# Kernel tuning notes

Measured on AMD Instinct MI355X. Metric: run time of the kernel, lower is better.

## Reference

```python
import jax, jax.numpy as jnp
import numpy as np

N_NODES = 100000
N_EDGES = 3200000
N_FEAT = 128
N_GRAPHS = 1024
N_CLASSES = 10
K = 30  # global_sort_pool k


def setup_inputs() -> dict:
    key = jax.random.key(0)
    ks = jax.random.split(key, 20)
    p = lambda k, shape: jax.random.normal(k, shape, jnp.float32) * 0.1
    return {
        "x": jax.random.normal(ks[0], (N_NODES, N_FEAT), jnp.float32),
        "w1": p(ks[1], (N_FEAT, 32)), "b1": p(ks[2], (32,)),
        "w2": p(ks[3], (32, 32)),     "b2": p(ks[4], (32,)),
        "w3": p(ks[5], (32, 32)),     "b3": p(ks[6], (32,)),
        "w4": p(ks[7], (32, 1)),      "b4": p(ks[8], (1,)),
        "conv5_w": p(ks[9], (16, 1, 97)),  "conv5_b": p(ks[10], (16,)),
        "conv6_w": p(ks[11], (32, 16, 5)), "conv6_b": p(ks[12], (32,)),
        "fc1_w": p(ks[13], (352, 128)),    "fc1_b": p(ks[14], (128,)),
        "fc2_w": p(ks[15], (128, N_CLASSES)), "fc2_b": p(ks[16], (N_CLASSES,)),
        "edge_src": jax.random.randint(ks[17], (N_EDGES,), 0, N_NODES),
        "edge_dst": jax.random.randint(ks[18], (N_EDGES,), 0, N_NODES),
        "batch": jnp.sort(jax.random.randint(ks[19], (N_NODES,), 0, N_GRAPHS)),
        "num_graphs": N_GRAPHS,
    }


def _gcn_forward(x, w1, b1, w2, b2, w3, b3, w4, b4,
                 conv5_w, conv5_b, conv6_w, conv6_b,
                 fc1_w, fc1_b, fc2_w, fc2_b,
                 edge_src, edge_dst, batch, num_graphs):
    n = x.shape[0]
    # remove_self_loops: mask self-loop edges to weight 0 (shapes stay static)
    ew = (edge_src != edge_dst).astype(x.dtype)
    # gcn_norm with added self-loops (weight 1): deg includes self-loop
    deg = jax.ops.segment_sum(ew, edge_dst, num_segments=n) + 1.0
    dis = jax.lax.rsqrt(deg)                       # deg^{-1/2}
    enorm = dis[edge_src] * dis[edge_dst] * ew     # [E]
    snorm = (dis * dis)[:, None]                   # self-loop norm [n,1]

    def gcn_conv(h, W, b):
        h = h @ W                                   # [n, out]
        agg = jax.ops.segment_sum(h[edge_src] * enorm[:, None], edge_dst,
                                  num_segments=n) + h * snorm
        return agg + b

    x1 = jnp.tanh(gcn_conv(x,  w1, b1))   # [n,32]
    x2 = jnp.tanh(gcn_conv(x1, w2, b2))   # [n,32]
    x3 = jnp.tanh(gcn_conv(x2, w3, b3))   # [n,32]
    x4 = jnp.tanh(gcn_conv(x3, w4, b4))   # [n,1]
    xc = jnp.concatenate([x1, x2, x3, x4], axis=-1)  # [n,97]

    # global_sort_pool(k=K): per-graph sort by last channel, descending
    key_last = xc[:, -1]
    order = jnp.lexsort((-key_last, batch))          # primary: batch, secondary: desc key
    bs = batch[order]                                # sorted graph ids
    counts = jax.ops.segment_sum(jnp.ones_like(batch, jnp.int32), batch,
                                 num_segments=num_graphs)
    starts = jnp.cumsum(counts) - counts             # exclusive prefix sum
    rank = jnp.arange(n) - starts[bs]                # rank within own graph
    r = jnp.where(rank < K, rank, K)                 # overflow -> dummy slot K
    pooled = jnp.zeros((num_graphs, K + 1, 97), xc.dtype)
    pooled = pooled.at[bs, r].set(xc[order])
    pooled = pooled[:, :K, :].reshape(num_graphs, 1, K * 97)  # [B,1,2910]

    # Conv1d(1,16,97,97) + relu
    h = jax.lax.conv_general_dilated(pooled, conv5_w, (97,), 'VALID',
                                     dimension_numbers=('NCH', 'OIH', 'NCH'))
    h = jax.nn.relu(h + conv5_b[None, :, None])      # [B,16,30]
    # MaxPool1d(2,2)
    h = jax.lax.reduce_window(h, -jnp.inf, jax.lax.max,
                              (1, 1, 2), (1, 1, 2), 'VALID')  # [B,16,15]
    # Conv1d(16,32,5,1) + relu
    h = jax.lax.conv_general_dilated(h, conv6_w, (1,), 'VALID',
                                     dimension_numbers=('NCH', 'OIH', 'NCH'))
    h = jax.nn.relu(h + conv6_b[None, :, None])      # [B,32,11]
    h = h.reshape(num_graphs, -1)                    # [B,352]

    h = jax.nn.relu(h @ fc1_w + fc1_b)               # [B,128]; dropout = identity (eval)
    return jax.nn.log_softmax(h @ fc2_w + fc2_b, axis=-1)  # [B,num_classes]


def reference(x, w1, b1, w2, b2, w3, b3, w4, b4,
              conv5_w, conv5_b, conv6_w, conv6_b,
              fc1_w, fc1_b, fc2_w, fc2_b,
              edge_src, edge_dst, batch, num_graphs):
    return _gcn_forward(x, w1, b1, w2, b2, w3, b3, w4, b4,
                        conv5_w, conv5_b, conv6_w, conv6_b,
                        fc1_w, fc1_b, fc2_w, fc2_b,
                        edge_src, edge_dst, batch, num_graphs)
```

## Files before the change

kernel.cpp:

```cpp
#include <hip/hip_runtime.h>
#include <hip/hip_bf16.h>

#define N_NODES 100000
#define N_EDGES 3200000
#define NGRAPH 1024
#define KTOP 30

#define NBKT 782
#define NTILE 391
#define TILE 8192
#define BKT_CAP 4736
#define GMAX 512

typedef __hip_bfloat16 bf16;
typedef float vfloat4 __attribute__((ext_vector_type(4)));

__device__ __forceinline__ float u2f(unsigned short h) {
    return __uint_as_float(((unsigned int)h) << 16);
}
__device__ __forceinline__ float LD(const void* p, int i, int bf) {
    if (bf) return u2f(((const unsigned short*)p)[i]);
    return ((const float*)p)[i];
}

__global__ void k_detect(const void* w1, int* flag) {
    if (threadIdx.x == 0 && blockIdx.x == 0) {
        const unsigned short* u = (const unsigned short*)w1;
        int plausible = 0;
        for (int i = 0; i < 64; i++) {
            float a = fabsf(u2f(u[2 * i]));
            if (a == 0.f || (a >= 9.765625e-4f && a <= 2.0f)) plausible++;
        }
        *flag = (plausible >= 40) ? 1 : 0;
    }
}

__global__ void k_icur(int* __restrict__ cur) {
    int i = blockIdx.x * 256 + threadIdx.x;
    if (i < NBKT) cur[i] = i * BKT_CAP;
}

__global__ __launch_bounds__(256) void k_scat(const int* __restrict__ src,
                                              const int* __restrict__ dst,
                                              int* __restrict__ cur,
                                              int* __restrict__ ebuf) {
    __shared__ int h[NBKT];
    __shared__ int base[NBKT];
    int tid = threadIdx.x;
    int ebase = blockIdx.x * TILE;
    for (int i = tid; i < NBKT; i += 256) h[i] = 0;
    __syncthreads();
    for (int i = tid; i < TILE; i += 256) {
        int e = ebase + i;
        if (e < N_EDGES) {
            int s = src[e], d = dst[e];
            if (s != d) atomicAdd(&h[d >> 7], 1);
        }
    }
    __syncthreads();
    for (int i = tid; i < NBKT; i += 256) {
        int c = h[i];
        base[i] = c ? atomicAdd(&cur[i], c) : 0;
    }
    __syncthreads();
    for (int i = tid; i < NBKT; i += 256) h[i] = 0;
    __syncthreads();
    for (int i = tid; i < TILE; i += 256) {
        int e = ebase + i;
        if (e < N_EDGES) {
            int s = src[e], d = dst[e];
            if (s != d) {
                int bkt = d >> 7;
                int p = base[bkt] + atomicAdd(&h[bkt], 1);
                if (p < (bkt + 1) * BKT_CAP) ebuf[p] = ((d & 127) << 17) | s;
            }
        }
    }
}

__global__ __launch_bounds__(256) void k_bcnt(const int* __restrict__ ebuf,
                                              const int* __restrict__ cur,
                                              int* __restrict__ rs,
                                              int* __restrict__ re,
                                              float* __restrict__ dis,
                                              int* __restrict__ deg) {
    __shared__ int dloc[128];
    __shared__ int sc[128];
    int b = blockIdx.x;
    int node0 = b << 7;
    int nn = N_NODES - node0; if (nn > 128) nn = 128;
    int tid = threadIdx.x;
    if (tid < 128) dloc[tid] = 0;
    __syncthreads();
    int s = b * BKT_CAP;
    int cnt = cur[b] - s; if (cnt > BKT_CAP) cnt = BKT_CAP;
    int e = s + cnt;
    for (int i = s + tid; i < e; i += 256)
        atomicAdd(&dloc[ebuf[i] >> 17], 1);
    __syncthreads();
    if (tid < 128) sc[tid] = dloc[tid];
    __syncthreads();
    for (int off = 1; off < 128; off <<= 1) {
        int t = (tid >= off && tid < 128) ? sc[tid - off] : 0;
        __syncthreads();
        if (tid < 128) sc[tid] += t;
        __syncthreads();
    }
    if (tid < nn) {
        int st = s + sc[tid] - dloc[tid];
        rs[node0 + tid] = st;
        re[node0 + tid] = st + dloc[tid];
        dis[node0 + tid] = rsqrtf((float)dloc[tid] + 1.0f);
        deg[node0 + tid] = dloc[tid];
    }
}

__global__ __launch_bounds__(256) void k_bfill(const int* __restrict__ ebuf,
                                               const int* __restrict__ cur,
                                               const int* __restrict__ rs,
                                               const int* __restrict__ deg,
                                               int* __restrict__ csr) {
    __shared__ int cl[128];
    int b = blockIdx.x;
    int node0 = b << 7;
    int tid = threadIdx.x;
    if (tid < 128) {
        int n = node0 + tid;
        cl[tid] = (n < N_NODES) ? rs[n] : 0;
    }
    __syncthreads();
    int s = b * BKT_CAP;
    int cnt = cur[b] - s; if (cnt > BKT_CAP) cnt = BKT_CAP;
    int e = s + cnt;
    for (int i = s + tid; i < e; i += 256) {
        int pv = ebuf[i];
        int srcn = pv & 0x1FFFF;
        int pos = atomicAdd(&cl[pv >> 17], 1);
        int d = deg[srcn];
        csr[pos] = (d << 17) | srcn;
    }
}

__global__ void k_gstart(const int* __restrict__ batch, int* __restrict__ gstart) {
    int g = blockIdx.x * 256 + threadIdx.x;
    if (g > NGRAPH) return;
    int lo = 0, hi = N_NODES;
    while (lo < hi) {
        int mid = (lo + hi) >> 1;
        if (batch[mid] < g) lo = mid + 1; else hi = mid;
    }
    gstart[g] = lo;
}

#define MM1_B 64
__global__ __launch_bounds__(256) void k_mm1(const void* __restrict__ x,
                                             const void* __restrict__ w,
                                             const int* __restrict__ flagp,
                                             const float* __restrict__ dis,
                                             float* __restrict__ ts) {
    __shared__ float Xs[MM1_B][129];
    __shared__ float Wf[128 * 32];
    int bf = *flagp;
    int tid = threadIdx.x;
    int nbase = blockIdx.x * MM1_B;
    if (bf) {
        const ushort4* wv = (const ushort4*)w;
        for (int idx = tid; idx < 1024; idx += 256) {
            ushort4 h = wv[idx];
            int p = idx * 4;
            Wf[p] = u2f(h.x); Wf[p + 1] = u2f(h.y); Wf[p + 2] = u2f(h.z); Wf[p + 3] = u2f(h.w);
        }
        const unsigned short* xb = (const unsigned short*)x;
        for (int idx = tid; idx < 1024; idx += 256) {
            int row = idx >> 4, c8 = (idx & 15) * 8;
            int gn = nbase + row; if (gn >= N_NODES) gn = N_NODES - 1;
            uint4 v = *(const uint4*)(xb + (size_t)gn * 128 + c8);
            float* d = &Xs[row][c8];
            d[0] = u2f((unsigned short)(v.x & 0xffff)); d[1] = u2f((unsigned short)(v.x >> 16));
            d[2] = u2f((unsigned short)(v.y & 0xffff)); d[3] = u2f((unsigned short)(v.y >> 16));
            d[4] = u2f((unsigned short)(v.z & 0xffff)); d[5] = u2f((unsigned short)(v.z >> 16));
            d[6] = u2f((unsigned short)(v.w & 0xffff)); d[7] = u2f((unsigned short)(v.w >> 16));
        }
    } else {
        const float* wf = (const float*)w;
        for (int idx = tid; idx < 4096; idx += 256) Wf[idx] = wf[idx];
        const float4* xv = (const float4*)x;
        for (int idx = tid; idx < 2048; idx += 256) {
            int row = idx >> 5, c4 = (idx & 31) * 4;
            int gn = nbase + row; if (gn >= N_NODES) gn = N_NODES - 1;
            float4 v = xv[(size_t)gn * 32 + (c4 >> 2)];
            float* d = &Xs[row][c4];
            d[0] = v.x; d[1] = v.y; d[2] = v.z; d[3] = v.w;
        }
    }
    __syncthreads();
    int tn = (tid & 15) * 4;
    int tc = (tid >> 4) * 2;
    float a00 = 0.f, a01 = 0.f, a10 = 0.f, a11 = 0.f;
    float a20 = 0.f, a21 = 0.f, a30 = 0.f, a31 = 0.f;
#pragma unroll 4
    for (int k = 0; k < 128; k++) {
        float2 wv = *(const float2*)&Wf[k * 32 + tc];
        float x0 = Xs[tn + 0][k], x1 = Xs[tn + 1][k];
        float x2 = Xs[tn + 2][k], x3 = Xs[tn + 3][k];
        a00 += x0 * wv.x; a01 += x0 * wv.y;
        a10 += x1 * wv.x; a11 += x1 * wv.y;
        a20 += x2 * wv.x; a21 += x2 * wv.y;
        a30 += x3 * wv.x; a31 += x3 * wv.y;
    }
    int n0 = nbase + tn;
    if (n0 + 0 < N_NODES) { float d = dis[n0 + 0]; *(float2*)&ts[(n0 + 0) * 32 + tc] = make_float2(d * a00, d * a01); }
    if (n0 + 1 < N_NODES) { float d = dis[n0 + 1]; *(float2*)&ts[(n0 + 1) * 32 + tc] = make_float2(d * a10, d * a11); }
    if (n0 + 2 < N_NODES) { float d = dis[n0 + 2]; *(float2*)&ts[(n0 + 2) * 32 + tc] = make_float2(d * a20, d * a21); }
    if (n0 + 3 < N_NODES) { float d = dis[n0 + 3]; *(float2*)&ts[(n0 + 3) * 32 + tc] = make_float2(d * a30, d * a31); }
}

__global__ __launch_bounds__(256) void k_agg(const float4* __restrict__ ts,
                                             const int* __restrict__ rs,
                                             const int* __restrict__ re,
                                             const int* __restrict__ csr,
                                             const float* __restrict__ dis,
                                             const void* __restrict__ b,
                                             const int* __restrict__ flagp,
                                             float4* __restrict__ out) {
    int node = blockIdx.x * 4 + (threadIdx.x >> 6);
    int lane = threadIdx.x & 63;
    int q   = lane & 7;
    int grp = lane >> 3;
    int bf = *flagp;
    int s = rs[node], e = re[node];
    float4 a0 = make_float4(0.f, 0.f, 0.f, 0.f);
    float4 a1 = a0, a2 = a0, a3 = a0;
    int i = s + grp;
    for (; i + 24 < e; i += 32) {
        int v0 = csr[i] & 0x1FFFF, v1 = csr[i + 8] & 0x1FFFF;
        int v2 = csr[i + 16] & 0x1FFFF, v3 = csr[i + 24] & 0x1FFFF;
        float4 m0 = ts[v0 * 8 + q];
        float4 m1 = ts[v1 * 8 + q];
        float4 m2 = ts[v2 * 8 + q];
        float4 m3 = ts[v3 * 8 + q];
        a0.x += m0.x; a0.y += m0.y; a0.z += m0.z; a0.w += m0.w;
        a1.x += m1.x; a1.y += m1.y; a1.z += m1.z; a1.w += m1.w;
        a2.x += m2.x; a2.y += m2.y; a2.z += m2.z; a2.w += m2.w;
        a3.x += m3.x; a3.y += m3.y; a3.z += m3.z; a3.w += m3.w;
    }
    for (; i < e; i += 8) {
        float4 m = ts[(csr[i] & 0x1FFFF) * 8 + q];
        a0.x += m.x; a0.y += m.y; a0.z += m.z; a0.w += m.w;
    }
    float4 acc;
    acc.x = (a0.x + a1.x) + (a2.x + a3.x);
    acc.y = (a0.y + a1.y) + (a2.y + a3.y);
    acc.z = (a0.z + a1.z) + (a2.z + a3.z);
    acc.w = (a0.w + a1.w) + (a2.w + a3.w);
#pragma unroll
    for (int off = 8; off < 64; off <<= 1) {
        acc.x += __shfl_xor(acc.x, off);
        acc.y += __shfl_xor(acc.y, off);
        acc.z += __shfl_xor(acc.z, off);
        acc.w += __shfl_xor(acc.w, off);
    }
    if (grp == 0) {
        float4 self = ts[node * 8 + q];
        float d = dis[node];
        vfloat4 r;
        r.x = tanhf(d * (acc.x + self.x) + LD(b, q * 4 + 0, bf));
        r.y = tanhf(d * (acc.y + self.y) + LD(b, q * 4 + 1, bf));
        r.z = tanhf(d * (acc.z + self.z) + LD(b, q * 4 + 2, bf));
        r.w = tanhf(d * (acc.w + self.w) + LD(b, q * 4 + 3, bf));
        __builtin_nontemporal_store(r, (vfloat4*)&out[node * 8 + q]);
    }
}

template<int DO_TS4>
__global__ __launch_bounds__(256) void k_aggz(const float4* __restrict__ xin,
                                              const int* __restrict__ rs,
                                              const int* __restrict__ re,
                                              const int* __restrict__ csr,
                                              const float* __restrict__ dis,
                                              const void* __restrict__ W,
                                              const void* __restrict__ b,
                                              const void* __restrict__ w4,
                                              const int* __restrict__ flagp,
                                              float* __restrict__ xout,
                                              float* __restrict__ ts4) {
    __shared__ float Wl[1024];
    __shared__ float W4l[32];
    __shared__ float Z[4][32];
    int tid = threadIdx.x;
    int bf = *flagp;
    if (bf) {
        ushort4 h = ((const ushort4*)W)[tid];
        int p = tid * 4;
        Wl[p] = u2f(h.x); Wl[p + 1] = u2f(h.y); Wl[p + 2] = u2f(h.z); Wl[p + 3] = u2f(h.w);
    } else {
        float4 v = ((const float4*)W)[tid];
        int p = tid * 4;
        Wl[p] = v.x; Wl[p + 1] = v.y; Wl[p + 2] = v.z; Wl[p + 3] = v.w;
    }
    if (DO_TS4 && tid < 32) W4l[tid] = LD(w4, tid, bf);

    int wid = tid >> 6;
    int node = blockIdx.x * 4 + wid;
    int lane = tid & 63;
    int q   = lane & 7;
    int grp = lane >> 3;
    int s = rs[node], e = re[node];
    float4 a0 = make_float4(0.f, 0.f, 0.f, 0.f);
    float4 a1 = a0, a2 = a0, a3 = a0;
    int i = s + grp;
    for (; i + 24 < e; i += 32) {
        int p0 = csr[i], p1 = csr[i + 8], p2 = csr[i + 16], p3 = csr[i + 24];
        int v0 = p0 & 0x1FFFF, v1 = p1 & 0x1FFFF, v2 = p2 & 0x1FFFF, v3 = p3 & 0x1FFFF;
        float d0 = rsqrtf((float)(p0 >> 17) + 1.0f);
        float d1 = rsqrtf((float)(p1 >> 17) + 1.0f);
        float d2 = rsqrtf((float)(p2 >> 17) + 1.0f);
        float d3 = rsqrtf((float)(p3 >> 17) + 1.0f);
        float4 m0 = xin[v0 * 8 + q];
        float4 m1 = xin[v1 * 8 + q];
        float4 m2 = xin[v2 * 8 + q];
        float4 m3 = xin[v3 * 8 + q];
        a0.x += d0 * m0.x; a0.y += d0 * m0.y; a0.z += d0 * m0.z; a0.w += d0 * m0.w;
        a1.x += d1 * m1.x; a1.y += d1 * m1.y; a1.z += d1 * m1.z; a1.w += d1 * m1.w;
        a2.x += d2 * m2.x; a2.y += d2 * m2.y; a2.z += d2 * m2.z; a2.w += d2 * m2.w;
        a3.x += d3 * m3.x; a3.y += d3 * m3.y; a3.z += d3 * m3.z; a3.w += d3 * m3.w;
    }
    for (; i < e; i += 8) {
        int pv = csr[i];
        int v = pv & 0x1FFFF;
        float dv = rsqrtf((float)(pv >> 17) + 1.0f);
        float4 m = xin[v * 8 + q];
        a0.x += dv * m.x; a0.y += dv * m.y; a0.z += dv * m.z; a0.w += dv * m.w;
    }
    float4 acc;
    acc.x = (a0.x + a1.x) + (a2.x + a3.x);
    acc.y = (a0.y + a1.y) + (a2.y + a3.y);
    acc.z = (a0.z + a1.z) + (a2.z + a3.z);
    acc.w = (a0.w + a1.w) + (a2.w + a3.w);
#pragma unroll
    for (int off = 8; off < 64; off <<= 1) {
        acc.x += __shfl_xor(acc.x, off);
        acc.y += __shfl_xor(acc.y, off);
        acc.z += __shfl_xor(acc.z, off);
        acc.w += __shfl_xor(acc.w, off);
    }
    if (grp == 0) {
        float4 self = xin[node * 8 + q];
        float di = dis[node];
        Z[wid][q * 4 + 0] = acc.x + di * self.x;
        Z[wid][q * 4 + 1] = acc.y + di * self.y;
        Z[wid][q * 4 + 2] = acc.z + di * self.z;
        Z[wid][q * 4 + 3] = acc.w + di * self.w;
    }
    __syncthreads();
    int nd = tid >> 6;
    int col = tid & 31;
    int kbase = (tid & 32) >> 1;
    const float* zr = Z[nd];
    float a = 0.f;
#pragma unroll
    for (int k2 = 0; k2 < 16; k2++) a += zr[kbase + k2] * Wl[(kbase + k2) * 32 + col];
    a += __shfl_xor(a, 32);
    int n2 = blockIdx.x * 4 + nd;
    float di2 = dis[n2];
    float xo = tanhf(di2 * a + LD(b, col, bf));
    if (!(tid & 32)) xout[n2 * 32 + col] = xo;
    if (DO_TS4) {
        float t4 = xo * W4l[col];
#pragma unroll
        for (int off = 1; off < 32; off <<= 1) t4 += __shfl_xor(t4, off);
        if ((tid & 63) == 0) ts4[n2] = di2 * t4;
    }
}

__global__ __launch_bounds__(256) void k_head(
    const float* __restrict__ x1, const float* __restrict__ x2,
    const float* __restrict__ x3, const float* __restrict__ ts4,
    const int* __restrict__ rs, const int* __restrict__ re,
    const int* __restrict__ csr, const float* __restrict__ dis,
    const int* __restrict__ gstart, const void* __restrict__ b4,
    const void* __restrict__ w5, const void* __restrict__ b5,
    const void* __restrict__ w6, const void* __restrict__ b6,
    const void* __restrict__ f1w, const void* __restrict__ f1b,
    const void* __restrict__ f2w, const void* __restrict__ f2b,
    const int* __restrict__ flagp, void* __restrict__ out) {
    __shared__ float P[KTOP * 100];
    __shared__ float W5[16 * 100];
    __shared__ float W6[32 * 16 * 5];
    __shared__ float H5[16][30];
    __shared__ float M[16][15];
    __shared__ float H6[352];
    __shared__ float Rp[256];
    __shared__ float R1[128];
    __shared__ float keys[GMAX];
    __shared__ int   selL[KTOP];
    __shared__ float L[10];
    __shared__ float mls;
    int g = blockIdx.x;
    int tid = threadIdx.x;
    int bf = *flagp;
    int s = gstart[g], e = gstart[g + 1];
    int gsize = e - s;
    int gl = gsize < GMAX ? gsize : GMAX;

    if (tid < KTOP) selL[tid] = -1;
    for (int i = tid; i < 16 * 97; i += 256) {
        int o = i / 97, f = i - o * 97;
        W5[o * 100 + f] = LD(w5, i, bf);
    }
    if (bf) {
        const ushort4* w6v = (const ushort4*)w6;
        for (int i = tid; i < 640; i += 256) {
            ushort4 h = w6v[i];
            int p = i * 4;
            W6[p] = u2f(h.x); W6[p + 1] = u2f(h.y); W6[p + 2] = u2f(h.z); W6[p + 3] = u2f(h.w);
        }
    } else {
        for (int i = tid; i < 2560; i += 256) W6[i] = ((const float*)w6)[i];
    }
    {
        int grp16 = tid >> 4;
        int ln16  = tid & 15;
        float b4v = LD(b4, 0, bf);
        for (int ln = grp16; ln < gl; ln += 16) {
            int node = s + ln;
            int st = rs[node], en = re[node];
            float acc = 0.f;
            for (int i = st + ln16; i < en; i += 16) acc += ts4[csr[i] & 0x1FFFF];
#pragma unroll
            for (int off = 1; off < 16; off <<= 1) acc += __shfl_xor(acc, off);
            if (ln16 == 0)
                keys[ln] = tanhf(dis[node] * (acc + ts4[node]) + b4v);
        }
    }
    __syncthreads();
    for (int li = tid; li < gl; li += 256) {
        float ki = keys[li];
        int rank = 0;
        for (int j = 0; j < gl; j++) {
            float kj = keys[j];
            rank += (kj > ki) || (kj == ki && j < li);
        }
        if (rank < KTOP) selL[rank] = li;
    }
    __syncthreads();
    for (int idx = tid; idx < KTOP * 97; idx += 256) {
        int p = idx / 97, f = idx - p * 97;
        int v = selL[p];
        float val = 0.f;
        if (v >= 0) {
            int gn = s + v;
            if (f < 32)      val = x1[gn * 32 + f];
            else if (f < 64) val = x2[gn * 32 + f - 32];
            else if (f < 96) val = x3[gn * 32 + f - 64];
            else             val = keys[v];
        }
        P[p * 100 + f] = val;
    }
    __syncthreads();
    for (int idx = tid; idx < 480; idx += 256) {
        int o = idx / 30, p = idx - o * 30;
        float acc = LD(b5, o, bf);
        const float* pr = &P[p * 100];
        const float* wr = &W5[o * 100];
#pragma unroll 6
        for (int f4 = 0; f4 < 24; f4++) {
            float4 a = *(const float4*)(pr + f4 * 4);
            float4 b = *(const float4*)(wr + f4 * 4);
            acc += b.x * a.x; acc += b.y * a.y; acc += b.z * a.z; acc += b.w * a.w;
        }
        acc += wr[96] * pr[96];
        H5[o][p] = fmaxf(acc, 0.f);
    }
    __syncthreads();
    for (int idx = tid; idx < 240; idx += 256) {
        int o = idx / 15, q = idx - o * 15;
        M[o][q] = fmaxf(H5[o][2 * q], H5[o][2 * q + 1]);
    }
    __syncthreads();
    for (int idx = tid; idx < 352; idx += 256) {
        int oc = idx / 11, tp = idx - oc * 11;
        float acc = LD(b6, oc, bf);
        const float* wr = &W6[oc * 80];
        for (int ic = 0; ic < 16; ic++) {
#pragma unroll
            for (int k = 0; k < 5; k++)
                acc += wr[ic * 5 + k] * M[ic][tp + k];
        }
        H6[idx] = fmaxf(acc, 0.f);
    }
    __syncthreads();
    {
        int half = tid >> 7, col = tid & 127;
        int base = half * 176;
        float a = 0.f;
        for (int i = 0; i < 176; i++) {
            int ii = base + i;
            a += H6[ii] * LD(f1w, ii * 128 + col, bf);
        }
        Rp[tid] = a;
    }
    __syncthreads();
    if (tid < 128) R1[tid] = fmaxf(LD(f1b, tid, bf) + Rp[tid] + Rp[128 + tid], 0.f);
    __syncthreads();
    if (tid < 10) {
        float acc = LD(f2b, tid, bf);
        for (int k = 0; k < 128; k++) acc += R1[k] * LD(f2w, k * 10 + tid, bf);
        L[tid] = acc;
    }
    __syncthreads();
    if (tid == 0) {
        float m = L[0];
        for (int c = 1; c < 10; c++) m = fmaxf(m, L[c]);
        float ssum = 0.f;
        for (int c = 0; c < 10; c++) ssum += expf(L[c] - m);
        mls = m + logf(ssum);
    }
    __syncthreads();
    if (tid < 10) {
        float v = L[tid] - mls;
        if (bf) ((bf16*)out)[g * 10 + tid] = __float2bfloat16(v);
        else    ((float*)out)[g * 10 + tid] = v;
    }
}

extern "C" void kernel_launch(void* const* d_in, const int* in_sizes, int n_in,
                              void* d_out, int out_size, void* d_ws, size_t ws_size,
                              hipStream_t stream) {
    const void* x   = d_in[0];
    const void* w1  = d_in[1];  const void* b1  = d_in[2];
    const void* w2  = d_in[3];  const void* b2  = d_in[4];
    const void* w3  = d_in[5];  const void* b3  = d_in[6];
    const void* w4  = d_in[7];  const void* b4  = d_in[8];
    const void* w5  = d_in[9];  const void* b5  = d_in[10];
    const void* w6  = d_in[11]; const void* b6  = d_in[12];
    const void* f1w = d_in[13]; const void* f1b = d_in[14];
    const void* f2w = d_in[15]; const void* f2b = d_in[16];
    const int* esrc  = (const int*)d_in[17];
    const int* edst  = (const int*)d_in[18];
    const int* batch = (const int*)d_in[19];

    char* w = (char*)d_ws;
    size_t off = 0;
    auto alloc = [&](size_t bytes) {
        void* p = w + off;
        off += (bytes + 255) & ~(size_t)255;
        return p;
    };
    int*   flag   = (int*)  alloc(256);
    int*   rs     = (int*)  alloc((size_t)N_NODES * 4);
    int*   re     = (int*)  alloc((size_t)N_NODES * 4);
    float* dis    = (float*)alloc((size_t)N_NODES * 4);
    int*   deg    = (int*)  alloc((size_t)N_NODES * 4);
    int*   csr    = (int*)  alloc((size_t)NBKT * BKT_CAP * 4);
    float* t      = (float*)alloc((size_t)N_NODES * 32 * 4);
    float* x1     = (float*)alloc((size_t)N_NODES * 32 * 4);
    float* x2     = (float*)alloc((size_t)N_NODES * 32 * 4);
    float* x3     = (float*)alloc((size_t)N_NODES * 32 * 4);
    float* ts4b   = (float*)alloc((size_t)N_NODES * 4);
    int*   gstart = (int*)  alloc((size_t)(NGRAPH + 1) * 4);
    int*   cur    = (int*)  alloc((size_t)NBKT * 4);
    (void)ws_size; (void)n_in; (void)in_sizes; (void)out_size;

    int* ebuf = (int*)t;

    int mb64 = (N_NODES + MM1_B - 1) / MM1_B;
    int ab   = N_NODES / 4;

    k_detect<<<1, 64, 0, stream>>>(w1, flag);
    k_icur<<<(NBKT + 255) / 256, 256, 0, stream>>>(cur);
    k_scat<<<NTILE, 256, 0, stream>>>(esrc, edst, cur, ebuf);
    k_bcnt<<<NBKT, 256, 0, stream>>>(ebuf, cur, rs, re, dis, deg);
    k_bfill<<<NBKT, 256, 0, stream>>>(ebuf, cur, rs, deg, csr);
    k_gstart<<<5, 256, 0, stream>>>(batch, gstart);

    k_mm1<<<mb64, 256, 0, stream>>>(x, w1, flag, dis, t);
    k_agg<<<ab, 256, 0, stream>>>((const float4*)t, rs, re, csr, dis, b1, flag, (float4*)x1);
    k_aggz<0><<<ab, 256, 0, stream>>>((const float4*)x1, rs, re, csr, dis, w2, b2, w4, flag, x2, ts4b);
    k_aggz<1><<<ab, 256, 0, stream>>>((const float4*)x2, rs, re, csr, dis, w3, b3, w4, flag, x3, ts4b);
    k_head<<<NGRAPH, 256, 0, stream>>>(x1, x2, x3, ts4b, rs, re, csr, dis,
                                       gstart, b4, w5, b5, w6, b6,
                                       f1w, f1b, f2w, f2b, flag, (void*)d_out);
}
```

Before: 542.5 us.

## Replace bucketed CSR build with global degree count, prefix scan and atomic fill

Swaps the two-pass bucket scatter (LDS histograms, per-bucket staging buffer, bucket-local count and fill) for a simpler CSR build. It counts per-node degree with global atomics, runs a three-stage prefix scan, then fills the CSR with per-node atomic cursors, reading edges as int4. This removes the staging buffer round trip and the fixed bucket capacity, but adds many scattered global atomics and writes with poor locality. It also unrolls the fc1 loop in the head kernel.

```diff
diff --git a/kernel.cpp b/kernel.cpp
--- a/kernel.cpp
+++ b/kernel.cpp
@@ -7,9 +7,6 @@
 #define KTOP 30
 
 #define NBKT 782
-#define NTILE 391
-#define TILE 8192
-#define BKT_CAP 4736
 #define GMAX 512
 
 typedef __hip_bfloat16 bf16;
@@ -35,110 +32,81 @@
     }
 }
 
-__global__ void k_icur(int* __restrict__ cur) {
+__global__ __launch_bounds__(256) void k_deg(const int4* __restrict__ src4,
+                                             const int4* __restrict__ dst4,
+                                             int* __restrict__ deg) {
     int i = blockIdx.x * 256 + threadIdx.x;
-    if (i < NBKT) cur[i] = i * BKT_CAP;
-}
-
-__global__ __launch_bounds__(256) void k_scat(const int* __restrict__ src,
-                                              const int* __restrict__ dst,
-                                              int* __restrict__ cur,
-                                              int* __restrict__ ebuf) {
-    __shared__ int h[NBKT];
-    __shared__ int base[NBKT];
-    int tid = threadIdx.x;
-    int ebase = blockIdx.x * TILE;
-    for (int i = tid; i < NBKT; i += 256) h[i] = 0;
-    __syncthreads();
-    for (int i = tid; i < TILE; i += 256) {
-        int e = ebase + i;
-        if (e < N_EDGES) {
-            int s = src[e], d = dst[e];
-            if (s != d) atomicAdd(&h[d >> 7], 1);
-        }
-    }
-    __syncthreads();
-    for (int i = tid; i < NBKT; i += 256) {
-        int c = h[i];
-        base[i] = c ? atomicAdd(&cur[i], c) : 0;
-    }
-    __syncthreads();
-    for (int i = tid; i < NBKT; i += 256) h[i] = 0;
-    __syncthreads();
-    for (int i = tid; i < TILE; i += 256) {
-        int e = ebase + i;
-        if (e < N_EDGES) {
-            int s = src[e], d = dst[e];
-            if (s != d) {
-                int bkt = d >> 7;
-                int p = base[bkt] + atomicAdd(&h[bkt], 1);
-                if (p < (bkt + 1) * BKT_CAP) ebuf[p] = ((d & 127) << 17) | s;
-            }
-        }
-    }
-}
-
-__global__ __launch_bounds__(256) void k_bcnt(const int* __restrict__ ebuf,
-                                              const int* __restrict__ cur,
+    if (i >= N_EDGES / 4) return;
+    int4 s = src4[i], d = dst4[i];
+    if (s.x != d.x) atomicAdd(&deg[d.x], 1);
+    if (s.y != d.y) atomicAdd(&deg[d.y], 1);
+    if (s.z != d.z) atomicAdd(&deg[d.z], 1);
+    if (s.w != d.w) atomicAdd(&deg[d.w], 1);
+}
+
+__global__ __launch_bounds__(128) void k_pfx1(const int* __restrict__ deg,
+                                              int* __restrict__ rs,
+                                              int* __restrict__ btot) {
+    __shared__ int sc[128];
+    int b = blockIdx.x, t = threadIdx.x;
+    int n = (b << 7) + t;
+    int v = (n < N_NODES) ? deg[n] : 0;
+    sc[t] = v;
+    __syncthreads();
+    for (int off = 1; off < 128; off <<= 1) {
+        int tv = (t >= off) ? sc[t - off] : 0;
+        __syncthreads();
+        sc[t] += tv;
+        __syncthreads();
+    }
+    if (n < N_NODES) rs[n] = sc[t] - v;
+    if (t == 127) btot[b] = sc[127];
+}
+
+__global__ __launch_bounds__(1024) void k_pfx2(const int* __restrict__ btot,
+                                               int* __restrict__ bstart) {
+    __shared__ int sh[1024];
+    int t = threadIdx.x;
+    int v = (t < NBKT) ? btot[t] : 0;
+    sh[t] = v;
+    __syncthreads();
+    for (int off = 1; off < 1024; off <<= 1) {
+        int tv = (t >= off) ? sh[t - off] : 0;
+        __syncthreads();
+        sh[t] += tv;
+        __syncthreads();
+    }
+    if (t < NBKT) bstart[t] = sh[t] - v;
+}
+
+__global__ __launch_bounds__(256) void k_pfx3(const int* __restrict__ deg,
+                                              const int* __restrict__ bstart,
                                               int* __restrict__ rs,
                                               int* __restrict__ re,
                                               float* __restrict__ dis,
-                                              int* __restrict__ deg) {
-    __shared__ int dloc[128];
-    __shared__ int sc[128];
-    int b = blockIdx.x;
-    int node0 = b << 7;
-    int nn = N_NODES - node0; if (nn > 128) nn = 128;
-    int tid = threadIdx.x;
-    if (tid < 128) dloc[tid] = 0;
-    __syncthreads();
-    int s = b * BKT_CAP;
-    int cnt = cur[b] - s; if (cnt > BKT_CAP) cnt = BKT_CAP;
-    int e = s + cnt;
-    for (int i = s + tid; i < e; i += 256)
-        atomicAdd(&dloc[ebuf[i] >> 17], 1);
-    __syncthreads();
-    if (tid < 128) sc[tid] = dloc[tid];
-    __syncthreads();
-    for (int off = 1; off < 128; off <<= 1) {
-        int t = (tid >= off && tid < 128) ? sc[tid - off] : 0;
-        __syncthreads();
-        if (tid < 128) sc[tid] += t;
-        __syncthreads();
-    }
-    if (tid < nn) {
-        int st = s + sc[tid] - dloc[tid];
-        rs[node0 + tid] = st;
-        re[node0 + tid] = st + dloc[tid];
-        dis[node0 + tid] = rsqrtf((float)dloc[tid] + 1.0f);
-        deg[node0 + tid] = dloc[tid];
-    }
-}
-
-__global__ __launch_bounds__(256) void k_bfill(const int* __restrict__ ebuf,
-                                               const int* __restrict__ cur,
-                                               const int* __restrict__ rs,
-                                               const int* __restrict__ deg,
-                                               int* __restrict__ csr) {
-    __shared__ int cl[128];
-    int b = blockIdx.x;
-    int node0 = b << 7;
-    int tid = threadIdx.x;
-    if (tid < 128) {
-        int n = node0 + tid;
-        cl[tid] = (n < N_NODES) ? rs[n] : 0;
-    }
-    __syncthreads();
-    int s = b * BKT_CAP;
-    int cnt = cur[b] - s; if (cnt > BKT_CAP) cnt = BKT_CAP;
-    int e = s + cnt;
-    for (int i = s + tid; i < e; i += 256) {
-        int pv = ebuf[i];
-        int srcn = pv & 0x1FFFF;
-        int pos = atomicAdd(&cl[pv >> 17], 1);
-        int d = deg[srcn];
-        csr[pos] = (d << 17) | srcn;
-    }
+                                              int* __restrict__ cur) {
+    int n = blockIdx.x * 256 + threadIdx.x;
+    if (n >= N_NODES) return;
+    int r = rs[n] + bstart[n >> 7];
+    int d = deg[n];
+    rs[n] = r;
+    re[n] = r + d;
+    dis[n] = rsqrtf((float)d + 1.0f);
+    cur[n] = r;
+}
+
+__global__ __launch_bounds__(256) void k_fill(const int4* __restrict__ src4,
+                                              const int4* __restrict__ dst4,
+                                              const int* __restrict__ deg,
+                                              int* __restrict__ cur,
+                                              int* __restrict__ csr) {
+    int i = blockIdx.x * 256 + threadIdx.x;
+    if (i >= N_EDGES / 4) return;
+    int4 s = src4[i], d = dst4[i];
+    if (s.x != d.x) { int p = atomicAdd(&cur[d.x], 1); csr[p] = (deg[s.x] << 17) | s.x; }
+    if (s.y != d.y) { int p = atomicAdd(&cur[d.y], 1); csr[p] = (deg[s.y] << 17) | s.y; }
+    if (s.z != d.z) { int p = atomicAdd(&cur[d.z], 1); csr[p] = (deg[s.z] << 17) | s.z; }
+    if (s.w != d.w) { int p = atomicAdd(&cur[d.w], 1); csr[p] = (deg[s.w] << 17) | s.w; }
 }
 
 __global__ void k_gstart(const int* __restrict__ batch, int* __restrict__ gstart) {
@@ -494,6 +462,7 @@
         int half = tid >> 7, col = tid & 127;
         int base = half * 176;
         float a = 0.f;
+#pragma unroll 8
         for (int i = 0; i < 176; i++) {
             int ii = base + i;
             a += H6[ii] * LD(f1w, ii * 128 + col, bf);
@@ -552,26 +521,30 @@
     int*   re     = (int*)  alloc((size_t)N_NODES * 4);
     float* dis    = (float*)alloc((size_t)N_NODES * 4);
     int*   deg    = (int*)  alloc((size_t)N_NODES * 4);
-    int*   csr    = (int*)  alloc((size_t)NBKT * BKT_CAP * 4);
+    int*   cur    = (int*)  alloc((size_t)N_NODES * 4);
+    int*   csr    = (int*)  alloc((size_t)N_EDGES * 4);
     float* t      = (float*)alloc((size_t)N_NODES * 32 * 4);
     float* x1     = (float*)alloc((size_t)N_NODES * 32 * 4);
     float* x2     = (float*)alloc((size_t)N_NODES * 32 * 4);
     float* x3     = (float*)alloc((size_t)N_NODES * 32 * 4);
     float* ts4b   = (float*)alloc((size_t)N_NODES * 4);
     int*   gstart = (int*)  alloc((size_t)(NGRAPH + 1) * 4);
-    int*   cur    = (int*)  alloc((size_t)NBKT * 4);
+    int*   btot   = (int*)  alloc((size_t)NBKT * 4);
+    int*   bstart = (int*)  alloc((size_t)NBKT * 4);
     (void)ws_size; (void)n_in; (void)in_sizes; (void)out_size;
 
-    int* ebuf = (int*)t;
-
+    (void)hipMemsetAsync(deg, 0, (size_t)N_NODES * 4, stream);
+
+    int eb4  = (N_EDGES / 4 + 255) / 256;
     int mb64 = (N_NODES + MM1_B - 1) / MM1_B;
     int ab   = N_NODES / 4;
 
     k_detect<<<1, 64, 0, stream>>>(w1, flag);
-    k_icur<<<(NBKT + 255) / 256, 256, 0, stream>>>(cur);
-    k_scat<<<NTILE, 256, 0, stream>>>(esrc, edst, cur, ebuf);
-    k_bcnt<<<NBKT, 256, 0, stream>>>(ebuf, cur, rs, re, dis, deg);
-    k_bfill<<<NBKT, 256, 0, stream>>>(ebuf, cur, rs, deg, csr);
+    k_deg<<<eb4, 256, 0, stream>>>((const int4*)esrc, (const int4*)edst, deg);
+    k_pfx1<<<NBKT, 128, 0, stream>>>(deg, rs, btot);
+    k_pfx2<<<1, 1024, 0, stream>>>(btot, bstart);
+    k_pfx3<<<(N_NODES + 255) / 256, 256, 0, stream>>>(deg, bstart, rs, re, dis, cur);
+    k_fill<<<eb4, 256, 0, stream>>>((const int4*)esrc, (const int4*)edst, deg, cur, csr);
     k_gstart<<<5, 256, 0, stream>>>(batch, gstart);
 
     k_mm1<<<mb64, 256, 0, stream>>>(x, w1, flag, dis, t);
```

New measurement: 803.6 us. 48.1% more time.

## Fuse CSR count and fill into cooperative kernel, merge init launches

Applied to the files above, without the earlier changes.

Merges the bucket count and bucket fill kernels into one cooperative-launch kernel. It stages each bucket's edges in shared memory and uses a grid-wide sync so that every block's degree is visible before the fill reads deg of source nodes. The gstart binary search is folded into the cursor init kernel, and the fc1 loop gets an unroll pragma. This removes two launches and one global re-read of ebuf, at the cost of requiring all 782 blocks (about 19KB LDS each) to be co-resident for the grid sync.

```diff
diff --git a/kernel.cpp b/kernel.cpp
--- a/kernel.cpp
+++ b/kernel.cpp
@@ -1,5 +1,8 @@
 #include <hip/hip_runtime.h>
 #include <hip/hip_bf16.h>
+#include <hip/hip_cooperative_groups.h>
+
+namespace cg = cooperative_groups;
 
 #define N_NODES 100000
 #define N_EDGES 3200000
@@ -35,9 +38,18 @@
     }
 }
 
-__global__ void k_icur(int* __restrict__ cur) {
+__global__ void k_init(const int* __restrict__ batch, int* __restrict__ gstart,
+                       int* __restrict__ cur) {
     int i = blockIdx.x * 256 + threadIdx.x;
     if (i < NBKT) cur[i] = i * BKT_CAP;
+    if (i <= NGRAPH) {
+        int lo = 0, hi = N_NODES;
+        while (lo < hi) {
+            int mid = (lo + hi) >> 1;
+            if (batch[mid] < i) lo = mid + 1; else hi = mid;
+        }
+        gstart[i] = lo;
+    }
 }
 
 __global__ __launch_bounds__(256) void k_scat(const int* __restrict__ src,
@@ -78,12 +90,14 @@
     }
 }
 
-__global__ __launch_bounds__(256) void k_bcnt(const int* __restrict__ ebuf,
-                                              const int* __restrict__ cur,
-                                              int* __restrict__ rs,
-                                              int* __restrict__ re,
-                                              float* __restrict__ dis,
-                                              int* __restrict__ deg) {
+__global__ __launch_bounds__(256) void k_bcsr2(const int* __restrict__ ebuf,
+                                               const int* __restrict__ cur,
+                                               int* __restrict__ rs,
+                                               int* __restrict__ re,
+                                               float* __restrict__ dis,
+                                               int* __restrict__ deg,
+                                               int* __restrict__ csr) {
+    __shared__ int stage[BKT_CAP];
     __shared__ int dloc[128];
     __shared__ int sc[128];
     int b = blockIdx.x;
@@ -94,9 +108,11 @@
     __syncthreads();
     int s = b * BKT_CAP;
     int cnt = cur[b] - s; if (cnt > BKT_CAP) cnt = BKT_CAP;
-    int e = s + cnt;
-    for (int i = s + tid; i < e; i += 256)
-        atomicAdd(&dloc[ebuf[i] >> 17], 1);
+    for (int i = tid; i < cnt; i += 256) {
+        int pv = ebuf[s + i];
+        stage[i] = pv;
+        atomicAdd(&dloc[pv >> 17], 1);
+    }
     __syncthreads();
     if (tid < 128) sc[tid] = dloc[tid];
     __syncthreads();
@@ -106,50 +122,27 @@
         if (tid < 128) sc[tid] += t;
         __syncthreads();
     }
+    int myrs = 0, mydeg = 0;
+    if (tid < 128) {
+        mydeg = dloc[tid];
+        myrs = s + sc[tid] - mydeg;
+    }
     if (tid < nn) {
-        int st = s + sc[tid] - dloc[tid];
-        rs[node0 + tid] = st;
-        re[node0 + tid] = st + dloc[tid];
-        dis[node0 + tid] = rsqrtf((float)dloc[tid] + 1.0f);
-        deg[node0 + tid] = dloc[tid];
-    }
-}
-
-__global__ __launch_bounds__(256) void k_bfill(const int* __restrict__ ebuf,
-                                               const int* __restrict__ cur,
-                                               const int* __restrict__ rs,
-                                               const int* __restrict__ deg,
-                                               int* __restrict__ csr) {
-    __shared__ int cl[128];
-    int b = blockIdx.x;
-    int node0 = b << 7;
-    int tid = threadIdx.x;
-    if (tid < 128) {
-        int n = node0 + tid;
-        cl[tid] = (n < N_NODES) ? rs[n] : 0;
-    }
-    __syncthreads();
-    int s = b * BKT_CAP;
-    int cnt = cur[b] - s; if (cnt > BKT_CAP) cnt = BKT_CAP;
-    int e = s + cnt;
-    for (int i = s + tid; i < e; i += 256) {
-        int pv = ebuf[i];
+        rs[node0 + tid] = myrs;
+        re[node0 + tid] = myrs + mydeg;
+        dis[node0 + tid] = rsqrtf((float)mydeg + 1.0f);
+        deg[node0 + tid] = mydeg;
+    }
+    __syncthreads();
+    if (tid < 128) dloc[tid] = myrs;
+    __threadfence();
+    cg::this_grid().sync();
+    for (int i = tid; i < cnt; i += 256) {
+        int pv = stage[i];
         int srcn = pv & 0x1FFFF;
-        int pos = atomicAdd(&cl[pv >> 17], 1);
-        int d = deg[srcn];
-        csr[pos] = (d << 17) | srcn;
-    }
-}
-
-__global__ void k_gstart(const int* __restrict__ batch, int* __restrict__ gstart) {
-    int g = blockIdx.x * 256 + threadIdx.x;
-    if (g > NGRAPH) return;
-    int lo = 0, hi = N_NODES;
-    while (lo < hi) {
-        int mid = (lo + hi) >> 1;
-        if (batch[mid] < g) lo = mid + 1; else hi = mid;
-    }
-    gstart[g] = lo;
+        int pos = atomicAdd(&dloc[pv >> 17], 1);
+        csr[pos] = (deg[srcn] << 17) | srcn;
+    }
 }
 
 #define MM1_B 64
@@ -494,6 +487,7 @@
         int half = tid >> 7, col = tid & 127;
         int base = half * 176;
         float a = 0.f;
+#pragma unroll 8
         for (int i = 0; i < 176; i++) {
             int ii = base + i;
             a += H6[ii] * LD(f1w, ii * 128 + col, bf);
@@ -568,11 +562,14 @@
     int ab   = N_NODES / 4;
 
     k_detect<<<1, 64, 0, stream>>>(w1, flag);
-    k_icur<<<(NBKT + 255) / 256, 256, 0, stream>>>(cur);
+    k_init<<<5, 256, 0, stream>>>(batch, gstart, cur);
     k_scat<<<NTILE, 256, 0, stream>>>(esrc, edst, cur, ebuf);
-    k_bcnt<<<NBKT, 256, 0, stream>>>(ebuf, cur, rs, re, dis, deg);
-    k_bfill<<<NBKT, 256, 0, stream>>>(ebuf, cur, rs, deg, csr);
-    k_gstart<<<5, 256, 0, stream>>>(batch, gstart);
+    {
+        void* cargs[] = {(void*)&ebuf, (void*)&cur, (void*)&rs, (void*)&re,
+                         (void*)&dis, (void*)&deg, (void*)&csr};
+        (void)hipLaunchCooperativeKernel((void*)k_bcsr2, dim3(NBKT), dim3(256),
+                                         cargs, 0, stream);
+    }
 
     k_mm1<<<mb64, 256, 0, stream>>>(x, w1, flag, dis, t);
     k_agg<<<ab, 256, 0, stream>>>((const float4*)t, rs, re, csr, dis, b1, flag, (float4*)x1);
```

After: 653.2 us. 20.4% more time.
